# Kernel tuning notes

Measured on AMD Instinct MI355X. Metric: run time of the kernel, lower is better.

## Reference

```python
import jax, jax.numpy as jnp
import numpy as np

# init_kwargs baked in as constants (defaults of OHLCVPackedScaler)
OPEN_IDX, HIGH_IDX, LOW_IDX, CLOSE_IDX = 0, 1, 2, 3
VOLUME_IDX, MINUTES_IDX, DOW_IDX = 4, 5, 6
CORRECTION = 1
MIN_SCALE = 1e-5


def _safe_div(numer, denom):
    # uni2ts safe_div: avoid div-by-zero, zero numer where denom==0 yields 0
    return numer / jnp.where(denom == 0, 1.0, denom)


def _group_id(variate_id):
    g = jnp.zeros_like(variate_id)
    ohlc = jnp.isin(variate_id, jnp.array([OPEN_IDX, HIGH_IDX, LOW_IDX, CLOSE_IDX]))
    g = jnp.where(ohlc, 0, g)
    g = jnp.where(variate_id == VOLUME_IDX, 1, g)
    g = jnp.where(variate_id == MINUTES_IDX, 2, g)
    g = jnp.where(variate_id == DOW_IDX, 3, g)
    return g


def setup_inputs() -> dict:
    key = jax.random.key(0)
    k1, k2, k3, k4 = jax.random.split(key, 4)
    B, S, D = 4, 4096, 32
    target = jax.random.normal(k1, (B, S, D), dtype=jnp.float32)
    observed_mask = jax.random.uniform(k2, (B, S, D)) < 0.9
    sample_id = jax.random.randint(k3, (B, S), 0, 8)   # 0 = padding
    variate_id = jax.random.randint(k4, (B, S), 0, 7)  # 0..6 per OHLCV layout
    return {"target": target, "observed_mask": observed_mask,
            "sample_id": sample_id, "variate_id": variate_id}


def reference(target, observed_mask, sample_id, variate_id):
    # original casts to double; we compute stats in fp32 (jax default) and return fp32
    t = target.astype(jnp.float32)
    obs = observed_mask.astype(t.dtype)
    gid = _group_id(variate_id)

    # pairwise (sample_id, group_id) equality mask  [B, S, S]
    id_mask = ((sample_id[..., :, None] == sample_id[..., None, :]) &
               (gid[..., :, None] == gid[..., None, :])).astype(t.dtype)

    # per-token sums over dim, then grouped sums via masked matvec
    tobs = jnp.einsum('bij,bj->bi', id_mask, jnp.sum(obs, axis=-1))[..., None]   # [B,S,1]
    loc = jnp.einsum('bij,bj->bi', id_mask, jnp.sum(t * obs, axis=-1))[..., None]
    loc = _safe_div(loc, tobs)

    var = jnp.einsum('bij,bj->bi', id_mask,
                     jnp.sum((t - loc) ** 2 * obs, axis=-1))[..., None]
    var = _safe_div(var, tobs - CORRECTION)
    scale = jnp.sqrt(var + MIN_SCALE)

    pad = (sample_id == 0)[..., None]
    loc = jnp.where(pad, 0.0, loc).astype(jnp.float32)
    scale = jnp.where(pad, 1.0, scale).astype(jnp.float32)
    return loc, scale
```

## Files before the change

### kernel.cpp

```cpp
#include <hip/hip_runtime.h>
#include <math.h>

#define BB 4
#define SS 4096
#define DD 32
#define NKEY 32
#define NSTAT 3
#define NTOK (BB * SS)


__global__ void ohlcv_init_detect(const unsigned char* __restrict__ mask_bytes,
                                  int* __restrict__ flag,
                                  float* __restrict__ acc) {
    int t = threadIdx.x;
    for (int i = t; i < BB * NKEY * NSTAT; i += blockDim.x) acc[i] = 0.0f;
    __shared__ int s_nz;
    if (t == 0) s_nz = 0;
    __syncthreads();
    if (t < 256) {
        if (mask_bytes[4 * t + 1] != 0) atomicOr(&s_nz, 1);
    }
    __syncthreads();
    if (t == 0) *flag = s_nz;
}

__global__ void ohlcv_accumulate(const float* __restrict__ target,
                                 const void* __restrict__ mask,
                                 const int* __restrict__ sample_id,
                                 const int* __restrict__ variate_id,
                                 const int* __restrict__ flag,
                                 float* __restrict__ acc) {
    __shared__ float s_acc[NKEY * NSTAT];
    int t = threadIdx.x;
    for (int i = t; i < NKEY * NSTAT; i += blockDim.x) s_acc[i] = 0.0f;
    __syncthreads();

    const int tokens_per_block = blockDim.x >> 5;
    int lt = t >> 5;
    int d  = t & 31;
    int token = blockIdx.x * tokens_per_block + lt;

    bool u8 = (*flag != 0);
    float tg = target[token * DD + d];
    bool obs;
    if (u8) obs = ((const unsigned char*)mask)[token * DD + d] != 0;
    else    obs = ((const int*)mask)[token * DD + d] != 0;

    float o  = obs ? 1.0f     : 0.0f;
    float x  = obs ? tg       : 0.0f;
    float x2 = obs ? tg * tg  : 0.0f;

    for (int off = 16; off > 0; off >>= 1) {
        o  += __shfl_down(o,  off, 32);
        x  += __shfl_down(x,  off, 32);
        x2 += __shfl_down(x2, off, 32);
    }

    if (d == 0) {
        int sid = sample_id[token];
        int vid = variate_id[token];
        int g   = (vid <= 3) ? 0 : (vid - 3);
        int key = sid * 4 + g;
        atomicAdd(&s_acc[key * NSTAT + 0], o);
        atomicAdd(&s_acc[key * NSTAT + 1], x);
        atomicAdd(&s_acc[key * NSTAT + 2], x2);
    }
    __syncthreads();

    int b = (blockIdx.x * tokens_per_block) / SS;
    for (int i = t; i < NKEY * NSTAT; i += blockDim.x) {
        float v = s_acc[i];
        if (v != 0.0f) atomicAdd(&acc[b * NKEY * NSTAT + i], v);
    }
}

__global__ void ohlcv_finalize(const int* __restrict__ sample_id,
                               const int* __restrict__ variate_id,
                               const float* __restrict__ acc,
                               float* __restrict__ out) {
    int token = blockIdx.x * blockDim.x + threadIdx.x;
    if (token >= NTOK) return;
    int b   = token / SS;
    int sid = sample_id[token];
    float loc, scale;
    if (sid == 0) {
        loc = 0.0f;
        scale = 1.0f;
    } else {
        int vid = variate_id[token];
        int g   = (vid <= 3) ? 0 : (vid - 3);
        int key = sid * 4 + g;
        const float* a = &acc[(b * NKEY + key) * NSTAT];
        float tobs  = a[0];
        float sum   = a[1];
        float sumsq = a[2];
        loc = sum / (tobs == 0.0f ? 1.0f : tobs);
        float varsum = sumsq - 2.0f * loc * sum + loc * loc * tobs;
        float denom  = tobs - 1.0f;
        float var    = varsum / (denom == 0.0f ? 1.0f : denom);
        scale = sqrtf(var + 1e-5f);
    }
    out[token] = loc;
    out[NTOK + token] = scale;
}

extern "C" void kernel_launch(void* const* d_in, const int* in_sizes, int n_in,
                              void* d_out, int out_size, void* d_ws, size_t ws_size,
                              hipStream_t stream) {
    const float* target      = (const float*)d_in[0];
    const void*  mask        = d_in[1];
    const int*   sample_id   = (const int*)d_in[2];
    const int*   variate_id  = (const int*)d_in[3];
    float*       out         = (float*)d_out;

    int*   flag = (int*)d_ws;
    float* acc  = (float*)((char*)d_ws + 16);

    ohlcv_init_detect<<<1, 512, 0, stream>>>((const unsigned char*)mask, flag, acc);

    int grid_acc = NTOK / 8;
    ohlcv_accumulate<<<grid_acc, 256, 0, stream>>>(target, mask, sample_id,
                                                   variate_id, flag, acc);

    int grid_fin = (NTOK + 255) / 256;
    ohlcv_finalize<<<grid_fin, 256, 0, stream>>>(sample_id, variate_id, acc, out);
}
```

Measured before the change: 78.95 us.

## Replace global atomics with per-block partials and fold init into accumulate

Drops the separate init/detect kernel. Each accumulate block now detects the mask dtype itself with a wavefront ballot. Blocks process 64 tokens instead of 8 and write a non-atomic partial stats row to the workspace. The finalize kernel then reduces its batch's 64 partial rows in shared memory before computing loc and scale. This removes a kernel launch and contended global atomics, at the cost of every finalize block redundantly summing the same batch's partials.

Result: faster. 68.85 us (-12.8%).

```diff
diff --git a/kernel.cpp b/kernel.cpp
--- a/kernel.cpp
+++ b/kernel.cpp
@@ -6,98 +6,94 @@
 #define DD 32
 #define NKEY 32
 #define NSTAT 3
+#define NPART (NKEY * NSTAT)
 #define NTOK (BB * SS)
+#define TOK_PER_B1 64
+#define NBLK1 (NTOK / TOK_PER_B1)
 
 
-__global__ void ohlcv_init_detect(const unsigned char* __restrict__ mask_bytes,
-                                  int* __restrict__ flag,
-                                  float* __restrict__ acc) {
+__global__ void ohlcv_partials(const float* __restrict__ target,
+                               const void* __restrict__ mask,
+                               const int* __restrict__ sample_id,
+                               const int* __restrict__ variate_id,
+                               float* __restrict__ partials) {
+    __shared__ float s_acc[NPART];
     int t = threadIdx.x;
-    for (int i = t; i < BB * NKEY * NSTAT; i += blockDim.x) acc[i] = 0.0f;
-    __shared__ int s_nz;
-    if (t == 0) s_nz = 0;
-    __syncthreads();
-    if (t < 256) {
-        if (mask_bytes[4 * t + 1] != 0) atomicOr(&s_nz, 1);
-    }
-    __syncthreads();
-    if (t == 0) *flag = s_nz;
-}
+    if (t < NPART) s_acc[t] = 0.0f;
 
-__global__ void ohlcv_accumulate(const float* __restrict__ target,
-                                 const void* __restrict__ mask,
-                                 const int* __restrict__ sample_id,
-                                 const int* __restrict__ variate_id,
-                                 const int* __restrict__ flag,
-                                 float* __restrict__ acc) {
-    __shared__ float s_acc[NKEY * NSTAT];
-    int t = threadIdx.x;
-    for (int i = t; i < NKEY * NSTAT; i += blockDim.x) s_acc[i] = 0.0f;
+    const unsigned char* mb = (const unsigned char*)mask;
+    int lane = t & 63;
+    bool u8 = (__ballot(mb[4 * lane + 1] != 0) != 0ULL);
     __syncthreads();
 
-    const int tokens_per_block = blockDim.x >> 5;
     int lt = t >> 5;
     int d  = t & 31;
-    int token = blockIdx.x * tokens_per_block + lt;
+    int base = blockIdx.x * TOK_PER_B1;
 
-    bool u8 = (*flag != 0);
-    float tg = target[token * DD + d];
-    bool obs;
-    if (u8) obs = ((const unsigned char*)mask)[token * DD + d] != 0;
-    else    obs = ((const int*)mask)[token * DD + d] != 0;
+    for (int k = 0; k < TOK_PER_B1 / 8; ++k) {
+        int token = base + k * 8 + lt;
+        float tg = target[token * DD + d];
+        bool obs;
+        if (u8) obs = ((const unsigned char*)mask)[token * DD + d] != 0;
+        else    obs = ((const int*)mask)[token * DD + d] != 0;
 
-    float o  = obs ? 1.0f     : 0.0f;
-    float x  = obs ? tg       : 0.0f;
-    float x2 = obs ? tg * tg  : 0.0f;
+        float o  = obs ? 1.0f    : 0.0f;
+        float x  = obs ? tg      : 0.0f;
+        float x2 = obs ? tg * tg : 0.0f;
 
-    for (int off = 16; off > 0; off >>= 1) {
-        o  += __shfl_down(o,  off, 32);
-        x  += __shfl_down(x,  off, 32);
-        x2 += __shfl_down(x2, off, 32);
-    }
+        for (int off = 16; off > 0; off >>= 1) {
+            o  += __shfl_down(o,  off, 32);
+            x  += __shfl_down(x,  off, 32);
+            x2 += __shfl_down(x2, off, 32);
+        }
 
-    if (d == 0) {
-        int sid = sample_id[token];
-        int vid = variate_id[token];
-        int g   = (vid <= 3) ? 0 : (vid - 3);
-        int key = sid * 4 + g;
-        atomicAdd(&s_acc[key * NSTAT + 0], o);
-        atomicAdd(&s_acc[key * NSTAT + 1], x);
-        atomicAdd(&s_acc[key * NSTAT + 2], x2);
+        if (d == 0) {
+            int sid = sample_id[token];
+            int vid = variate_id[token];
+            int g   = (vid <= 3) ? 0 : (vid - 3);
+            int key = (sid * 4 + g) * NSTAT;
+            atomicAdd(&s_acc[key + 0], o);
+            atomicAdd(&s_acc[key + 1], x);
+            atomicAdd(&s_acc[key + 2], x2);
+        }
     }
     __syncthreads();
 
-    int b = (blockIdx.x * tokens_per_block) / SS;
-    for (int i = t; i < NKEY * NSTAT; i += blockDim.x) {
-        float v = s_acc[i];
-        if (v != 0.0f) atomicAdd(&acc[b * NKEY * NSTAT + i], v);
-    }
+    if (t < NPART) partials[blockIdx.x * NPART + t] = s_acc[t];
 }
 
 __global__ void ohlcv_finalize(const int* __restrict__ sample_id,
                                const int* __restrict__ variate_id,
-                               const float* __restrict__ acc,
+                               const float* __restrict__ partials,
                                float* __restrict__ out) {
-    int token = blockIdx.x * blockDim.x + threadIdx.x;
-    if (token >= NTOK) return;
-    int b   = token / SS;
+    __shared__ float s_fin[NPART];
+    int t = threadIdx.x;
+    int b = (blockIdx.x * 256) / SS;
+
+    if (t < NPART) {
+        const float* p = partials + (size_t)b * (NBLK1 / BB) * NPART + t;
+        float s = 0.0f;
+        #pragma unroll 8
+        for (int q = 0; q < NBLK1 / BB; ++q) s += p[q * NPART];
+        s_fin[t] = s;
+    }
+    __syncthreads();
+
+    int token = blockIdx.x * 256 + t;
     int sid = sample_id[token];
-    float loc, scale;
-    if (sid == 0) {
-        loc = 0.0f;
-        scale = 1.0f;
-    } else {
+    float loc = 0.0f, scale = 1.0f;
+    if (sid != 0) {
         int vid = variate_id[token];
         int g   = (vid <= 3) ? 0 : (vid - 3);
-        int key = sid * 4 + g;
-        const float* a = &acc[(b * NKEY + key) * NSTAT];
-        float tobs  = a[0];
-        float sum   = a[1];
-        float sumsq = a[2];
-        loc = sum / (tobs == 0.0f ? 1.0f : tobs);
-        float varsum = sumsq - 2.0f * loc * sum + loc * loc * tobs;
+        int key = (sid * 4 + g) * NSTAT;
+        float tobs  = s_fin[key + 0];
+        float sum   = s_fin[key + 1];
+        float sumsq = s_fin[key + 2];
+        float l = sum / (tobs == 0.0f ? 1.0f : tobs);
+        float varsum = sumsq - 2.0f * l * sum + l * l * tobs;
         float denom  = tobs - 1.0f;
         float var    = varsum / (denom == 0.0f ? 1.0f : denom);
+        loc = l;
         scale = sqrtf(var + 1e-5f);
     }
     out[token] = loc;
@@ -107,21 +103,15 @@
 extern "C" void kernel_launch(void* const* d_in, const int* in_sizes, int n_in,
                               void* d_out, int out_size, void* d_ws, size_t ws_size,
                               hipStream_t stream) {
-    const float* target      = (const float*)d_in[0];
-    const void*  mask        = d_in[1];
-    const int*   sample_id   = (const int*)d_in[2];
-    const int*   variate_id  = (const int*)d_in[3];
-    float*       out         = (float*)d_out;
+    const float* target     = (const float*)d_in[0];
+    const void*  mask       = d_in[1];
+    const int*   sample_id  = (const int*)d_in[2];
+    const int*   variate_id = (const int*)d_in[3];
+    float*       out        = (float*)d_out;
+    float*       partials   = (float*)d_ws;
 
-    int*   flag = (int*)d_ws;
-    float* acc  = (float*)((char*)d_ws + 16);
-
-    ohlcv_init_detect<<<1, 512, 0, stream>>>((const unsigned char*)mask, flag, acc);
-
-    int grid_acc = NTOK / 8;
-    ohlcv_accumulate<<<grid_acc, 256, 0, stream>>>(target, mask, sample_id,
-                                                   variate_id, flag, acc);
-
-    int grid_fin = (NTOK + 255) / 256;
-    ohlcv_finalize<<<grid_fin, 256, 0, stream>>>(sample_id, variate_id, acc, out);
+    ohlcv_partials<<<NBLK1, 256, 0, stream>>>(target, mask, sample_id,
+                                              variate_id, partials);
+    ohlcv_finalize<<<NTOK / 256, 256, 0, stream>>>(sample_id, variate_id,
+                                                   partials, out);
 }
```
